# Optimization experiments

Hardware: AMD Instinct MI355X
Metric: run time of the kernel (lower is better)

The kernel has to match this reference:

```python
import jax, jax.numpy as jnp
import numpy as np

N_TH1 = 30
LB = 1e-20
UB = 1e20
LB_EXP = -20.0
UB_EXP = 20.0


def make_directions(n_th1):
    # Reproduces the TF __init__ direction sampling on the sphere.
    n_th2 = 2 * (n_th1 - 1) + 1
    th1 = np.linspace(-np.pi / 2, np.pi / 2, n_th1)
    th2 = np.linspace(-np.pi, np.pi, n_th2)
    c1, s1 = np.cos(th1), np.sin(th1)
    c2, s2 = np.cos(th2), np.sin(th2)
    dx = np.outer(c1[1:-1], c2[:-1])          # [n_th1-2, n_th2-1]
    dy = np.outer(c1[1:-1], s2[:-1])
    dz = np.broadcast_to(s1[1:-1, None], dx.shape)
    mid = np.stack([dx, dy, dz], -1).reshape(-1, 3)
    poles = np.array([[c1[0] * c2[0], c1[0] * s2[0], s1[0]],
                      [c1[-1] * c2[0], c1[-1] * s2[0], s1[-1]]])
    return np.concatenate([mid, poles], 0).astype(np.float32)  # [D, 3]


def setup_inputs() -> dict:
    key = jax.random.key(0)
    k1, k2, k3 = jax.random.split(key, 3)
    vertices = jax.random.normal(k1, (8, 64, 32, 3), jnp.float32)
    # smoothness is a p-norm exponent; realistic range [2, 20]
    smoothness = 2.0 + 18.0 * jax.random.uniform(k2, (8, 64), jnp.float32)
    pointcloud = jax.random.normal(k3, (8, 2048, 3), jnp.float32)
    return {"vertices": vertices, "smoothness": smoothness, "pointcloud": pointcloud}


def _spt_forward(vertices, smoothness):
    dirs = jnp.asarray(make_directions(N_TH1))            # [D, 3]
    B, P = vertices.shape[0], vertices.shape[1]
    mean_v = jnp.mean(vertices, axis=2, keepdims=True)    # [B,P,1,3]
    local_v = vertices - mean_v                           # [B,P,V,3]

    # z = <v, x> for every vertex/direction pair -> [B,P,V,D]
    z = jnp.einsum('bpvc,dc->bpvd', local_v, dirs)
    zm = jnp.maximum(z, 0.0)
    p = smoothness[:, :, None, None]                      # [B,P,1,1]

    # dynamic rescaling k = 10^ceil(...) to keep zm^p in fp range
    zm_max = jnp.max(zm, axis=2, keepdims=True)           # [B,P,1,D]
    zm_log = jnp.log(zm_max) / jnp.log(10.0)              # = max over V of log10(zm)
    exponent = zm_log * p
    lk = jnp.where(exponent < LB_EXP, (-15.0 - exponent) / p, 0.0)
    k = 10.0 ** jnp.clip(jnp.ceil(lk), 0.0, UB_EXP)       # [B,P,1,D]
    k = jax.lax.stop_gradient(k)                          # ceil has zero grad anyway

    zm = zm * k
    pos = zm > 0
    # clip(zm^p, lb, ub) - (zm==0)*lb  ==  where(zm>0, clip(zm^p,lb,ub), 0)
    zm_p = jnp.where(pos, jnp.clip(jnp.where(pos, zm, 1.0) ** p, LB, UB), 0.0)
    sum_zm_p = jnp.sum(zm_p, axis=2, keepdims=True)       # [B,P,1,D]
    spos = sum_zm_p > 0
    h = jnp.where(spos, jnp.clip(jnp.where(spos, sum_zm_p, 1.0) ** (1.0 / p), LB, UB), LB)

    # dh/dz = clip((zm/h)^(p-1), lb, ub)
    ratio = zm / h                                        # [B,P,V,D]
    rpos = ratio > 0
    dhdz = jnp.where(rpos, jnp.clip(jnp.where(rpos, ratio, 1.0) ** (p - 1.0), LB, UB), LB)
    # dh/dx = dhdz^T @ vertices -> surface points
    dhdx = jnp.einsum('bpvd,bpvc->bpdc', dhdz, local_v)   # [B,P,D,3]
    surf = dhdx + mean_v                                  # broadcast [B,P,1,3]

    h_out = jnp.clip(h / k, -UB, UB)                      # [B,P,1,D]
    h_out = jnp.transpose(h_out, (0, 1, 3, 2))            # [B,P,D,1]
    local_dirs = jnp.broadcast_to(dirs[None, None], (B, P) + dirs.shape)
    direction_h = jnp.concatenate([local_dirs, h_out], axis=-1)  # [B,P,D,4]
    points = surf.reshape(B, -1, 3)                       # [B, P*D, 3]
    mean_out = mean_v.reshape(B, P, 3)
    return points, direction_h, mean_out, local_v


def reference(vertices, smoothness, pointcloud):
    points, direction_h, mean_out, local_v = _spt_forward(vertices, smoothness)
    B, P = vertices.shape[0], vertices.shape[1]
    # overlap / retraction loops are truncated in the source; placeholders
    overlap = jnp.zeros((B, P, 1), jnp.float32)
    retraction = jnp.zeros((B, P, 1), jnp.float32)
    return (points, direction_h, overlap, retraction, mean_out, local_v)
```

## Files before the change

### kernel.cpp

```cpp
#include <hip/hip_runtime.h>
#include <math.h>

#define NBP 512
#define VV 32
#define DD 1626
#define DHALF 813

#define O_POINTS 0
#define O_DIRH   2497536
#define O_OVER   5827584
#define O_RETR   5828096
#define O_MEAN   5828608
#define O_LOCAL  5830144

#define L10_2 0.3010299956639812f
#define L2_10 3.321928094887362f
#define LH_MIN -66.43856189774725f

__device__ __forceinline__ float fexp2(float x) {
  return __builtin_amdgcn_exp2f(x);
}

__device__ __forceinline__ void make_dir_fast(int d, float& x, float& y, float& z) {
  if (d < 1624) {
    const int i1 = d / 58 + 1;
    const int i2 = d - (i1 - 1) * 58;
    const float STEP = 0.10833078115826873f;
    const float th1 = -1.5707963267948966f + (float)i1 * STEP;
    const float th2 = -3.14159265358979323846f + (float)i2 * STEP;
    const float s1 = __sinf(th1);
    const float c1 = __cosf(th1);
    const float s2 = __sinf(th2);
    const float c2 = __cosf(th2);
    x = c1 * c2; y = c1 * s2; z = s1;
  } else if (d == 1624) {
    x = -6.123234e-17f; y = -7.49880e-33f; z = -1.0f;
  } else {
    x = -6.123234e-17f; y = -7.49880e-33f; z = 1.0f;
  }
}

__global__ __launch_bounds__(256) void spt_kernel(
    const float* __restrict__ vertices,
    const float* __restrict__ smooth,
    float* __restrict__ out)
{
  const int bp   = blockIdx.x;
  const int half = blockIdx.y;
  const int tid  = threadIdx.x;

  __shared__ __align__(16) float slvx[VV];
  __shared__ __align__(16) float slvy[VV];
  __shared__ __align__(16) float slvz[VV];

  const int dbase = half * DHALF;

  const int v = tid & 31;
  const float* vp = vertices + bp * (VV * 3) + v * 3;
  const float vx = vp[0], vy = vp[1], vz = vp[2];
  float sx = vx, sy = vy, sz = vz;
#pragma unroll
  for (int m = 16; m >= 1; m >>= 1) {
    sx += __shfl_xor(sx, m);
    sy += __shfl_xor(sy, m);
    sz += __shfl_xor(sz, m);
  }
  const float mx = sx * (1.0f / 32.0f);
  const float my = sy * (1.0f / 32.0f);
  const float mz = sz * (1.0f / 32.0f);
  if (tid < VV) {
    slvx[tid] = vx - mx;
    slvy[tid] = vy - my;
    slvz[tid] = vz - mz;
  }
  __syncthreads();

  if (half == 1) {
    if (tid < VV * 3) {
      const int vv = tid / 3, c = tid - vv * 3;
      const float val = (c == 0) ? slvx[vv] : ((c == 1) ? slvy[vv] : slvz[vv]);
      out[O_LOCAL + bp * (VV * 3) + tid] = val;
    }
    if (tid == 96) {
      out[O_MEAN + bp * 3 + 0] = mx;
      out[O_MEAN + bp * 3 + 1] = my;
      out[O_MEAN + bp * 3 + 2] = mz;
      out[O_OVER + bp] = 0.f;
      out[O_RETR + bp] = 0.f;
    }
  }

  const float p     = smooth[bp];
  const float inv_p = 1.0f / p;
  const float pm1   = p - 1.0f;
  const float plt   = p * L10_2;

  const float4* lvx4 = (const float4*)slvx;
  const float4* lvy4 = (const float4*)slvy;
  const float4* lvz4 = (const float4*)slvz;

  auto process = [&](int idx) {
    const int d = dbase + idx;
    float dx, dy, dz;
    make_dir_fast(d, dx, dy, dz);

    float w[VV];
    float zmax = 0.f;
#pragma unroll
    for (int j = 0; j < VV / 4; j++) {
      float4 X = lvx4[j], Y = lvy4[j], Z = lvz4[j];
      float z0 = fmaxf(fmaf(X.x, dx, fmaf(Y.x, dy, Z.x * dz)), 0.f);
      float z1 = fmaxf(fmaf(X.y, dx, fmaf(Y.y, dy, Z.y * dz)), 0.f);
      float z2 = fmaxf(fmaf(X.z, dx, fmaf(Y.z, dy, Z.z * dz)), 0.f);
      float z3 = fmaxf(fmaf(X.w, dx, fmaf(Y.w, dy, Z.w * dz)), 0.f);
      w[j * 4 + 0] = z0; w[j * 4 + 1] = z1;
      w[j * 4 + 2] = z2; w[j * 4 + 3] = z3;
      zmax = fmaxf(zmax, fmaxf(fmaxf(z0, z1), fmaxf(z2, z3)));
    }

    const float expo = __log2f(zmax) * plt;
    float kc = 0.f;
    if (expo < -20.f) {
      kc = fminf(fmaxf(ceilf((-15.f - expo) * inv_p), 0.f), 20.f);
    }
    const float kcl = kc * L2_10;
    const float A   = p * kcl;

    float s0 = 0.f, s1 = 0.f, s2 = 0.f, s3 = 0.f;
#pragma unroll
    for (int j = 0; j < VV / 4; j++) {
      float z0 = w[j * 4 + 0], z1 = w[j * 4 + 1];
      float z2 = w[j * 4 + 2], z3 = w[j * 4 + 3];
      float w0 = fexp2(fmaf(pm1, __log2f(z0), A));
      float w1 = fexp2(fmaf(pm1, __log2f(z1), A));
      float w2 = fexp2(fmaf(pm1, __log2f(z2), A));
      float w3 = fexp2(fmaf(pm1, __log2f(z3), A));
      s0 += w0 * z0;  s1 += w1 * z1;
      s2 += w2 * z2;  s3 += w3 * z3;
      w[j * 4 + 0] = w0; w[j * 4 + 1] = w1;
      w[j * 4 + 2] = w2; w[j * 4 + 3] = w3;
    }
    const float ssum = (s0 + s1) + (s2 + s3);

    float lh = LH_MIN;
    float C2 = 0.f;
    if (ssum > 0.f) {
      lh = inv_p * __log2f(ssum);
      C2 = fexp2(-fmaf(pm1, lh, kcl));
    }

    float ax = 0.f, ay = 0.f, az = 0.f;
#pragma unroll
    for (int j = 0; j < VV / 4; j++) {
      float4 X = lvx4[j], Y = lvy4[j], Z = lvz4[j];
      float w0 = w[j * 4 + 0], w1 = w[j * 4 + 1];
      float w2 = w[j * 4 + 2], w3 = w[j * 4 + 3];
      ax = fmaf(w0, X.x, fmaf(w1, X.y, fmaf(w2, X.z, fmaf(w3, X.w, ax))));
      ay = fmaf(w0, Y.x, fmaf(w1, Y.y, fmaf(w2, Y.z, fmaf(w3, Y.w, ay))));
      az = fmaf(w0, Z.x, fmaf(w1, Z.y, fmaf(w2, Z.z, fmaf(w3, Z.w, az))));
    }

    const int pbase = bp * DD + d;
    out[O_POINTS + pbase * 3 + 0] = fmaf(C2, ax, mx);
    out[O_POINTS + pbase * 3 + 1] = fmaf(C2, ay, my);
    out[O_POINTS + pbase * 3 + 2] = fmaf(C2, az, mz);

    float4 dvh = make_float4(dx, dy, dz, fexp2(lh - kcl));
    ((float4*)(out + O_DIRH))[pbase] = dvh;
  };

  process(tid);
  process(256 + tid);
  process(512 + tid);
  if (tid < DHALF - 768) process(768 + tid);
}

extern "C" void kernel_launch(void* const* d_in, const int* in_sizes, int n_in,
                              void* d_out, int out_size, void* d_ws, size_t ws_size,
                              hipStream_t stream) {
  const float* vertices = (const float*)d_in[0];
  const float* smooth   = (const float*)d_in[1];
  float* out = (float*)d_out;

  spt_kernel<<<dim3(NBP, 2), 256, 0, stream>>>(vertices, smooth, out);
}
```

Baseline: 77.09 us.

## Cache local vertices in registers, recompute projections, fuse weight and accumulation loops

Loads the 32 centered vertices from shared memory into 96 per-thread registers once, instead of re-reading them from LDS in every direction iteration. The per-direction w[32] array is dropped: projections are recomputed in a second pass, and the weighted-sum loop is merged with the surface-point accumulation. A launch-bounds occupancy hint of 3 is also added. The goal is fewer LDS reads and less register-array pressure, at the cost of 96 extra FMAs per direction and a large persistent register footprint.

```diff
diff --git a/kernel.cpp b/kernel.cpp
--- a/kernel.cpp
+++ b/kernel.cpp
@@ -40,7 +40,7 @@
   }
 }
 
-__global__ __launch_bounds__(256) void spt_kernel(
+__global__ __launch_bounds__(256, 3) void spt_kernel(
     const float* __restrict__ vertices,
     const float* __restrict__ smooth,
     float* __restrict__ out)
@@ -90,33 +90,38 @@
     }
   }
 
+  float lx[VV], ly[VV], lz[VV];
+#pragma unroll
+  for (int j = 0; j < VV / 4; j++) {
+    const float4 X = ((const float4*)slvx)[j];
+    const float4 Y = ((const float4*)slvy)[j];
+    const float4 Z = ((const float4*)slvz)[j];
+    lx[4*j+0] = X.x; lx[4*j+1] = X.y; lx[4*j+2] = X.z; lx[4*j+3] = X.w;
+    ly[4*j+0] = Y.x; ly[4*j+1] = Y.y; ly[4*j+2] = Y.z; ly[4*j+3] = Y.w;
+    lz[4*j+0] = Z.x; lz[4*j+1] = Z.y; lz[4*j+2] = Z.z; lz[4*j+3] = Z.w;
+  }
+
   const float p     = smooth[bp];
   const float inv_p = 1.0f / p;
   const float pm1   = p - 1.0f;
   const float plt   = p * L10_2;
-
-  const float4* lvx4 = (const float4*)slvx;
-  const float4* lvy4 = (const float4*)slvy;
-  const float4* lvz4 = (const float4*)slvz;
 
   auto process = [&](int idx) {
     const int d = dbase + idx;
     float dx, dy, dz;
     make_dir_fast(d, dx, dy, dz);
 
-    float w[VV];
-    float zmax = 0.f;
+    float zm0 = 0.f, zm1 = 0.f, zm2 = 0.f, zm3 = 0.f;
 #pragma unroll
     for (int j = 0; j < VV / 4; j++) {
-      float4 X = lvx4[j], Y = lvy4[j], Z = lvz4[j];
-      float z0 = fmaxf(fmaf(X.x, dx, fmaf(Y.x, dy, Z.x * dz)), 0.f);
-      float z1 = fmaxf(fmaf(X.y, dx, fmaf(Y.y, dy, Z.y * dz)), 0.f);
-      float z2 = fmaxf(fmaf(X.z, dx, fmaf(Y.z, dy, Z.z * dz)), 0.f);
-      float z3 = fmaxf(fmaf(X.w, dx, fmaf(Y.w, dy, Z.w * dz)), 0.f);
-      w[j * 4 + 0] = z0; w[j * 4 + 1] = z1;
-      w[j * 4 + 2] = z2; w[j * 4 + 3] = z3;
-      zmax = fmaxf(zmax, fmaxf(fmaxf(z0, z1), fmaxf(z2, z3)));
+      float z0 = fmaxf(fmaf(lx[4*j+0], dx, fmaf(ly[4*j+0], dy, lz[4*j+0] * dz)), 0.f);
+      float z1 = fmaxf(fmaf(lx[4*j+1], dx, fmaf(ly[4*j+1], dy, lz[4*j+1] * dz)), 0.f);
+      float z2 = fmaxf(fmaf(lx[4*j+2], dx, fmaf(ly[4*j+2], dy, lz[4*j+2] * dz)), 0.f);
+      float z3 = fmaxf(fmaf(lx[4*j+3], dx, fmaf(ly[4*j+3], dy, lz[4*j+3] * dz)), 0.f);
+      zm0 = fmaxf(zm0, z0); zm1 = fmaxf(zm1, z1);
+      zm2 = fmaxf(zm2, z2); zm3 = fmaxf(zm3, z3);
     }
+    const float zmax = fmaxf(fmaxf(zm0, zm1), fmaxf(zm2, zm3));
 
     const float expo = __log2f(zmax) * plt;
     float kc = 0.f;
@@ -127,18 +132,22 @@
     const float A   = p * kcl;
 
     float s0 = 0.f, s1 = 0.f, s2 = 0.f, s3 = 0.f;
+    float ax = 0.f, ay = 0.f, az = 0.f;
 #pragma unroll
     for (int j = 0; j < VV / 4; j++) {
-      float z0 = w[j * 4 + 0], z1 = w[j * 4 + 1];
-      float z2 = w[j * 4 + 2], z3 = w[j * 4 + 3];
+      float z0 = fmaxf(fmaf(lx[4*j+0], dx, fmaf(ly[4*j+0], dy, lz[4*j+0] * dz)), 0.f);
+      float z1 = fmaxf(fmaf(lx[4*j+1], dx, fmaf(ly[4*j+1], dy, lz[4*j+1] * dz)), 0.f);
+      float z2 = fmaxf(fmaf(lx[4*j+2], dx, fmaf(ly[4*j+2], dy, lz[4*j+2] * dz)), 0.f);
+      float z3 = fmaxf(fmaf(lx[4*j+3], dx, fmaf(ly[4*j+3], dy, lz[4*j+3] * dz)), 0.f);
       float w0 = fexp2(fmaf(pm1, __log2f(z0), A));
       float w1 = fexp2(fmaf(pm1, __log2f(z1), A));
       float w2 = fexp2(fmaf(pm1, __log2f(z2), A));
       float w3 = fexp2(fmaf(pm1, __log2f(z3), A));
       s0 += w0 * z0;  s1 += w1 * z1;
       s2 += w2 * z2;  s3 += w3 * z3;
-      w[j * 4 + 0] = w0; w[j * 4 + 1] = w1;
-      w[j * 4 + 2] = w2; w[j * 4 + 3] = w3;
+      ax = fmaf(w0, lx[4*j+0], fmaf(w1, lx[4*j+1], fmaf(w2, lx[4*j+2], fmaf(w3, lx[4*j+3], ax))));
+      ay = fmaf(w0, ly[4*j+0], fmaf(w1, ly[4*j+1], fmaf(w2, ly[4*j+2], fmaf(w3, ly[4*j+3], ay))));
+      az = fmaf(w0, lz[4*j+0], fmaf(w1, lz[4*j+1], fmaf(w2, lz[4*j+2], fmaf(w3, lz[4*j+3], az))));
     }
     const float ssum = (s0 + s1) + (s2 + s3);
 
@@ -147,17 +156,6 @@
     if (ssum > 0.f) {
       lh = inv_p * __log2f(ssum);
       C2 = fexp2(-fmaf(pm1, lh, kcl));
-    }
-
-    float ax = 0.f, ay = 0.f, az = 0.f;
-#pragma unroll
-    for (int j = 0; j < VV / 4; j++) {
-      float4 X = lvx4[j], Y = lvy4[j], Z = lvz4[j];
-      float w0 = w[j * 4 + 0], w1 = w[j * 4 + 1];
-      float w2 = w[j * 4 + 2], w3 = w[j * 4 + 3];
-      ax = fmaf(w0, X.x, fmaf(w1, X.y, fmaf(w2, X.z, fmaf(w3, X.w, ax))));
-      ay = fmaf(w0, Y.x, fmaf(w1, Y.y, fmaf(w2, Y.z, fmaf(w3, Y.w, ay))));
-      az = fmaf(w0, Z.x, fmaf(w1, Z.y, fmaf(w2, Z.z, fmaf(w3, Z.w, az))));
     }
 
     const int pbase = bp * DD + d;
```

Result: slower. 112.9 us (+46.4%).

## Broadcast vertices via readlane into SGPRs and recompute z instead of storing

Applied to the files above, without the earlier changes.

Local vertex coordinates are kept in registers and broadcast to uniform scalar values with readlane, which removes the shared-memory staging, the barrier and the LDS reads in the inner loops. The per-direction work is restructured into two passes: the first finds zmax, the second recomputes z and accumulates the weighted sums and surface point together. This drops the 32-element per-thread array that had to stay live across phases. The cost is 96 uniform values held in scalar registers plus recomputed dot products, which adds some VALU work and puts pressure on the scalar register file.

```diff
diff --git a/kernel.cpp b/kernel.cpp
--- a/kernel.cpp
+++ b/kernel.cpp
@@ -40,6 +40,68 @@
   }
 }
 
+#define RL(x, i) __uint_as_float(__builtin_amdgcn_readlane(__float_as_uint(x), (i)))
+
+#define DECL_CHUNK(b)                                                       \
+  const float cx_##b##_0 = RL(lvx, 4*b+0), cx_##b##_1 = RL(lvx, 4*b+1),     \
+              cx_##b##_2 = RL(lvx, 4*b+2), cx_##b##_3 = RL(lvx, 4*b+3);     \
+  const float cy_##b##_0 = RL(lvy, 4*b+0), cy_##b##_1 = RL(lvy, 4*b+1),     \
+              cy_##b##_2 = RL(lvy, 4*b+2), cy_##b##_3 = RL(lvy, 4*b+3);     \
+  const float cz_##b##_0 = RL(lvz, 4*b+0), cz_##b##_1 = RL(lvz, 4*b+1),     \
+              cz_##b##_2 = RL(lvz, 4*b+2), cz_##b##_3 = RL(lvz, 4*b+3);
+
+#define P1CH(b) {                                                           \
+  float z0 = fmaxf(fmaf(cx_##b##_0, dx, fmaf(cy_##b##_0, dy, cz_##b##_0 * dz)), 0.f); \
+  float z1 = fmaxf(fmaf(cx_##b##_1, dx, fmaf(cy_##b##_1, dy, cz_##b##_1 * dz)), 0.f); \
+  float z2 = fmaxf(fmaf(cx_##b##_2, dx, fmaf(cy_##b##_2, dy, cz_##b##_2 * dz)), 0.f); \
+  float z3 = fmaxf(fmaf(cx_##b##_3, dx, fmaf(cy_##b##_3, dy, cz_##b##_3 * dz)), 0.f); \
+  zm0 = fmaxf(zm0, z0); zm1 = fmaxf(zm1, z1);                               \
+  zm2 = fmaxf(zm2, z2); zm3 = fmaxf(zm3, z3); }
+
+#define P2CH(b) {                                                           \
+  float z0 = fmaxf(fmaf(cx_##b##_0, dx, fmaf(cy_##b##_0, dy, cz_##b##_0 * dz)), 0.f); \
+  float z1 = fmaxf(fmaf(cx_##b##_1, dx, fmaf(cy_##b##_1, dy, cz_##b##_1 * dz)), 0.f); \
+  float z2 = fmaxf(fmaf(cx_##b##_2, dx, fmaf(cy_##b##_2, dy, cz_##b##_2 * dz)), 0.f); \
+  float z3 = fmaxf(fmaf(cx_##b##_3, dx, fmaf(cy_##b##_3, dy, cz_##b##_3 * dz)), 0.f); \
+  float w0 = fexp2(fmaf(pm1, __log2f(z0), A));                              \
+  float w1 = fexp2(fmaf(pm1, __log2f(z1), A));                              \
+  float w2 = fexp2(fmaf(pm1, __log2f(z2), A));                              \
+  float w3 = fexp2(fmaf(pm1, __log2f(z3), A));                              \
+  s0 += w0 * z0;  s1 += w1 * z1;                                            \
+  s2 += w2 * z2;  s3 += w3 * z3;                                            \
+  ax = fmaf(w0, cx_##b##_0, fmaf(w1, cx_##b##_1, fmaf(w2, cx_##b##_2, fmaf(w3, cx_##b##_3, ax)))); \
+  ay = fmaf(w0, cy_##b##_0, fmaf(w1, cy_##b##_1, fmaf(w2, cy_##b##_2, fmaf(w3, cy_##b##_3, ay)))); \
+  az = fmaf(w0, cz_##b##_0, fmaf(w1, cz_##b##_1, fmaf(w2, cz_##b##_2, fmaf(w3, cz_##b##_3, az)))); }
+
+#define PROCESS(IDX) do {                                                   \
+  const int d = dbase + (IDX);                                              \
+  float dx, dy, dz;                                                         \
+  make_dir_fast(d, dx, dy, dz);                                             \
+  float zm0 = 0.f, zm1 = 0.f, zm2 = 0.f, zm3 = 0.f;                         \
+  P1CH(0) P1CH(1) P1CH(2) P1CH(3) P1CH(4) P1CH(5) P1CH(6) P1CH(7)           \
+  const float zmax = fmaxf(fmaxf(zm0, zm1), fmaxf(zm2, zm3));               \
+  const float expo = __log2f(zmax) * plt;                                   \
+  float kc = 0.f;                                                           \
+  if (expo < -20.f) kc = fminf(fmaxf(ceilf((-15.f - expo) * inv_p), 0.f), 20.f); \
+  const float kcl = kc * L2_10;                                             \
+  const float A   = p * kcl;                                                \
+  float s0 = 0.f, s1 = 0.f, s2 = 0.f, s3 = 0.f;                             \
+  float ax = 0.f, ay = 0.f, az = 0.f;                                       \
+  P2CH(0) P2CH(1) P2CH(2) P2CH(3) P2CH(4) P2CH(5) P2CH(6) P2CH(7)           \
+  const float ssum = (s0 + s1) + (s2 + s3);                                 \
+  float lh = LH_MIN, C2 = 0.f;                                              \
+  if (ssum > 0.f) {                                                         \
+    lh = inv_p * __log2f(ssum);                                             \
+    C2 = fexp2(-fmaf(pm1, lh, kcl));                                        \
+  }                                                                         \
+  const int pbase = bp * DD + d;                                            \
+  out[O_POINTS + pbase * 3 + 0] = fmaf(C2, ax, mx);                         \
+  out[O_POINTS + pbase * 3 + 1] = fmaf(C2, ay, my);                         \
+  out[O_POINTS + pbase * 3 + 2] = fmaf(C2, az, mz);                         \
+  float4 dvh = make_float4(dx, dy, dz, fexp2(lh - kcl));                    \
+  ((float4*)(out + O_DIRH))[pbase] = dvh;                                   \
+} while (0)
+
 __global__ __launch_bounds__(256) void spt_kernel(
     const float* __restrict__ vertices,
     const float* __restrict__ smooth,
@@ -48,10 +110,6 @@
   const int bp   = blockIdx.x;
   const int half = blockIdx.y;
   const int tid  = threadIdx.x;
-
-  __shared__ __align__(16) float slvx[VV];
-  __shared__ __align__(16) float slvy[VV];
-  __shared__ __align__(16) float slvz[VV];
 
   const int dbase = half * DHALF;
 
@@ -68,18 +126,19 @@
   const float mx = sx * (1.0f / 32.0f);
   const float my = sy * (1.0f / 32.0f);
   const float mz = sz * (1.0f / 32.0f);
-  if (tid < VV) {
-    slvx[tid] = vx - mx;
-    slvy[tid] = vy - my;
-    slvz[tid] = vz - mz;
-  }
-  __syncthreads();
+
+  const float lvx = vx - mx;
+  const float lvy = vy - my;
+  const float lvz = vz - mz;
+
+  DECL_CHUNK(0) DECL_CHUNK(1) DECL_CHUNK(2) DECL_CHUNK(3)
+  DECL_CHUNK(4) DECL_CHUNK(5) DECL_CHUNK(6) DECL_CHUNK(7)
 
   if (half == 1) {
-    if (tid < VV * 3) {
-      const int vv = tid / 3, c = tid - vv * 3;
-      const float val = (c == 0) ? slvx[vv] : ((c == 1) ? slvy[vv] : slvz[vv]);
-      out[O_LOCAL + bp * (VV * 3) + tid] = val;
+    if (tid < VV) {
+      out[O_LOCAL + bp * (VV * 3) + tid * 3 + 0] = lvx;
+      out[O_LOCAL + bp * (VV * 3) + tid * 3 + 1] = lvy;
+      out[O_LOCAL + bp * (VV * 3) + tid * 3 + 2] = lvz;
     }
     if (tid == 96) {
       out[O_MEAN + bp * 3 + 0] = mx;
@@ -95,84 +154,10 @@
   const float pm1   = p - 1.0f;
   const float plt   = p * L10_2;
 
-  const float4* lvx4 = (const float4*)slvx;
-  const float4* lvy4 = (const float4*)slvy;
-  const float4* lvz4 = (const float4*)slvz;
-
-  auto process = [&](int idx) {
-    const int d = dbase + idx;
-    float dx, dy, dz;
-    make_dir_fast(d, dx, dy, dz);
-
-    float w[VV];
-    float zmax = 0.f;
-#pragma unroll
-    for (int j = 0; j < VV / 4; j++) {
-      float4 X = lvx4[j], Y = lvy4[j], Z = lvz4[j];
-      float z0 = fmaxf(fmaf(X.x, dx, fmaf(Y.x, dy, Z.x * dz)), 0.f);
-      float z1 = fmaxf(fmaf(X.y, dx, fmaf(Y.y, dy, Z.y * dz)), 0.f);
-      float z2 = fmaxf(fmaf(X.z, dx, fmaf(Y.z, dy, Z.z * dz)), 0.f);
-      float z3 = fmaxf(fmaf(X.w, dx, fmaf(Y.w, dy, Z.w * dz)), 0.f);
-      w[j * 4 + 0] = z0; w[j * 4 + 1] = z1;
-      w[j * 4 + 2] = z2; w[j * 4 + 3] = z3;
-      zmax = fmaxf(zmax, fmaxf(fmaxf(z0, z1), fmaxf(z2, z3)));
-    }
-
-    const float expo = __log2f(zmax) * plt;
-    float kc = 0.f;
-    if (expo < -20.f) {
-      kc = fminf(fmaxf(ceilf((-15.f - expo) * inv_p), 0.f), 20.f);
-    }
-    const float kcl = kc * L2_10;
-    const float A   = p * kcl;
-
-    float s0 = 0.f, s1 = 0.f, s2 = 0.f, s3 = 0.f;
-#pragma unroll
-    for (int j = 0; j < VV / 4; j++) {
-      float z0 = w[j * 4 + 0], z1 = w[j * 4 + 1];
-      float z2 = w[j * 4 + 2], z3 = w[j * 4 + 3];
-      float w0 = fexp2(fmaf(pm1, __log2f(z0), A));
-      float w1 = fexp2(fmaf(pm1, __log2f(z1), A));
-      float w2 = fexp2(fmaf(pm1, __log2f(z2), A));
-      float w3 = fexp2(fmaf(pm1, __log2f(z3), A));
-      s0 += w0 * z0;  s1 += w1 * z1;
-      s2 += w2 * z2;  s3 += w3 * z3;
-      w[j * 4 + 0] = w0; w[j * 4 + 1] = w1;
-      w[j * 4 + 2] = w2; w[j * 4 + 3] = w3;
-    }
-    const float ssum = (s0 + s1) + (s2 + s3);
-
-    float lh = LH_MIN;
-    float C2 = 0.f;
-    if (ssum > 0.f) {
-      lh = inv_p * __log2f(ssum);
-      C2 = fexp2(-fmaf(pm1, lh, kcl));
-    }
-
-    float ax = 0.f, ay = 0.f, az = 0.f;
-#pragma unroll
-    for (int j = 0; j < VV / 4; j++) {
-      float4 X = lvx4[j], Y = lvy4[j], Z = lvz4[j];
-      float w0 = w[j * 4 + 0], w1 = w[j * 4 + 1];
-      float w2 = w[j * 4 + 2], w3 = w[j * 4 + 3];
-      ax = fmaf(w0, X.x, fmaf(w1, X.y, fmaf(w2, X.z, fmaf(w3, X.w, ax))));
-      ay = fmaf(w0, Y.x, fmaf(w1, Y.y, fmaf(w2, Y.z, fmaf(w3, Y.w, ay))));
-      az = fmaf(w0, Z.x, fmaf(w1, Z.y, fmaf(w2, Z.z, fmaf(w3, Z.w, az))));
-    }
-
-    const int pbase = bp * DD + d;
-    out[O_POINTS + pbase * 3 + 0] = fmaf(C2, ax, mx);
-    out[O_POINTS + pbase * 3 + 1] = fmaf(C2, ay, my);
-    out[O_POINTS + pbase * 3 + 2] = fmaf(C2, az, mz);
-
-    float4 dvh = make_float4(dx, dy, dz, fexp2(lh - kcl));
-    ((float4*)(out + O_DIRH))[pbase] = dvh;
-  };
-
-  process(tid);
-  process(256 + tid);
-  process(512 + tid);
-  if (tid < DHALF - 768) process(768 + tid);
+  PROCESS(tid);
+  PROCESS(256 + tid);
+  PROCESS(512 + tid);
+  if (tid < DHALF - 768) PROCESS(768 + tid);
 }
 
 extern "C" void kernel_launch(void* const* d_in, const int* in_sizes, int n_in,
```

Result: no change. 75.69 us, median of 2 (-1.8%).
